# Kernel tuning notes

Hardware: AMD Instinct MI355X
Metric: run time of the kernel (lower is better)

Reference implementation:

```python
import jax, jax.numpy as jnp
import numpy as np

H = 1024        # hidden_dim
MD = 2048       # memory_dim
L = 16384       # memory length == max_length
N = 8           # head_N
# sys.float_info.min underflows to 0.0 in float32, exactly as in the torch
# original (python float * float32 tensor). Kept for faithfulness.
TINY = jnp.float32(2.2250738585072014e-308)


def setup_inputs() -> dict:
    key = jax.random.key(0)
    ks = jax.random.split(key, 12)
    s_h = 1.0 / np.sqrt(H)
    s_m = 1.0 / np.sqrt(MD)
    s_o = 1.0 / np.sqrt(2 * H)
    return {
        "x": jax.random.normal(ks[0], (1, 1, H), jnp.float32),
        "memory": jax.random.normal(ks[1], (L, MD), jnp.float32),
        "Wq": jax.random.uniform(ks[2], (H, H), jnp.float32, -s_h, s_h),
        "bq": jax.random.uniform(ks[3], (H,), jnp.float32, -s_h, s_h),
        "Wk": jax.random.uniform(ks[4], (H, MD), jnp.float32, -s_m, s_m),
        "bk": jax.random.uniform(ks[5], (H,), jnp.float32, -s_m, s_m),
        "Wv": jax.random.uniform(ks[6], (H, MD), jnp.float32, -s_m, s_m),
        "bv": jax.random.uniform(ks[7], (H,), jnp.float32, -s_m, s_m),
        "Wo": jax.random.uniform(ks[8], (H, 2 * H), jnp.float32, -s_o, s_o),
        "bo": jax.random.uniform(ks[9], (H,), jnp.float32, -s_o, s_o),
    }


def reference(x, memory, Wq, bq, Wk, bk, Wv, bv, Wo, bo):
    d = H // N  # per-head dim
    # Q: (1,H) -> (1,d,N) -> (N,1,d), scaled by d**-0.5
    q = x.reshape(1, -1) @ Wq.T + bq
    Q = q.reshape(1, d, N).transpose(2, 0, 1) * (d ** -0.5)
    # K: (L,H) -> (L,d,N) -> (N,d,L)
    K = (memory @ Wk.T + bk).reshape(-1, d, N).transpose(2, 1, 0)
    QK = jnp.einsum('nod,ndl->nol', Q, K)  # (N,1,L)
    # pad mask: 1 where the memory row sums to zero, else 0 (as in torch nonzero-set)
    any_zero = memory.sum(axis=1)
    pad_mask = (any_zero == 0).astype(QK.dtype)[None, None, :]
    QK = QK + pad_mask * TINY
    attn = jax.nn.softmax(QK, axis=-1)
    # V: (L,H) -> (L,d,N) -> (N,L,d)
    V = (memory @ Wv.T + bv).reshape(-1, d, N).transpose(2, 0, 1)
    feat = jnp.einsum('nol,nld->nod', attn, V)      # (N,1,d)
    feat = feat.transpose(1, 2, 0).reshape(1, 1, H)  # (1,1,H)
    ax = jnp.concatenate([x, feat], axis=-1)         # (1,1,2H)
    return jax.nn.relu(ax @ Wo.T + bo)
```

## Files before the change

### kernel.cpp

```cpp
#include <hip/hip_runtime.h>
#include <math.h>

#define HDIM  1024
#define MDIM  2048
#define RSQRT_D 0.08838834764831844f

#define OFF_W     0
#define OFF_BETA  16384
#define OFF_Z     16392
#define OFF_Q     16400
#define OFF_FEAT  17424
#define OFF_Y     18448
#define OFF_ZP    34832
#define OFF_YBUF  301072

__device__ __forceinline__ float dot4(float4 a, float4 b) {
  return a.x * b.x + a.y * b.y + a.z * b.z + a.w * b.w;
}
__device__ __forceinline__ void fma4(float4& acc, float s, float4 v) {
  acc.x = fmaf(s, v.x, acc.x); acc.y = fmaf(s, v.y, acc.y);
  acc.z = fmaf(s, v.z, acc.z); acc.w = fmaf(s, v.w, acc.w);
}
__device__ __forceinline__ void add4(float4& a, float4 v) {
  a.x += v.x; a.y += v.y; a.z += v.z; a.w += v.w;
}

__global__ __launch_bounds__(256) void kq(const float* __restrict__ x,
                                          const float* __restrict__ Wq,
                                          const float* __restrict__ bq,
                                          float* __restrict__ ws) {
  int tid = threadIdx.x, lane = tid & 63;
  int j = blockIdx.x * 4 + (tid >> 6);
  const float4* xr = (const float4*)x;
  const float4* wr = (const float4*)(Wq + (size_t)j * HDIM);
  float acc = 0.f;
#pragma unroll
  for (int i = 0; i < 4; ++i) {
    int idx = i * 64 + lane;
    acc += dot4(xr[idx], wr[idx]);
  }
#pragma unroll
  for (int off = 32; off; off >>= 1) acc += __shfl_xor(acc, off);
  if (lane == 0) ws[OFF_Q + j] = acc + bq[j];
  if (tid < 64) ws[OFF_W + blockIdx.x * 64 + tid] = 0.f;
}

__global__ __launch_bounds__(256) void kw(const float* __restrict__ Wk,
                                          const float* __restrict__ bk,
                                          float* __restrict__ ws) {
  __shared__ float lds[32];
  int tid = threadIdx.x;
  const float* q = ws + OFF_Q;
  if (blockIdx.x == 256) {
    float b = 0.f;
#pragma unroll
    for (int i = 0; i < 4; ++i) {
      int c = tid + 256 * i;
      b = fmaf(q[c], bk[c], b);
    }
    b += __shfl_xor(b, 8); b += __shfl_xor(b, 16); b += __shfl_xor(b, 32);
    if ((tid & 63) < 8) lds[(tid >> 6) * 8 + (tid & 7)] = b;
    __syncthreads();
    if (tid < 8)
      ws[OFF_BETA + tid] = lds[tid] + lds[8 + tid] + lds[16 + tid] + lds[24 + tid];
    return;
  }
  int mc = blockIdx.x & 7, cc = blockIdx.x >> 3;
  int m = mc * 256 + tid;
  float acc[8];
#pragma unroll
  for (int n = 0; n < 8; ++n) acc[n] = 0.f;
  int c0 = cc * 32;
#pragma unroll
  for (int cb = 0; cb < 32; cb += 8) {
#pragma unroll
    for (int u = 0; u < 8; ++u)
      acc[u] = fmaf(q[c0 + cb + u], Wk[(size_t)(c0 + cb + u) * MDIM + m], acc[u]);
  }
#pragma unroll
  for (int n = 0; n < 8; ++n) atomicAdd(&ws[OFF_W + n * MDIM + m], acc[n]);
}

__global__ __launch_bounds__(512, 4) void kab(const float* __restrict__ mem,
                                              float* __restrict__ ws) {
  __shared__ float4 wlds[4096];
  __shared__ __align__(16) float pp[256];
  __shared__ float zz[64];
  __shared__ float bb[8];
  int tid = threadIdx.x, lane = tid & 63, wv = tid >> 6;
  int bid = blockIdx.x;
  int r0 = bid * 32;

  const float4* wsrc = (const float4*)(ws + OFF_W);
#pragma unroll
  for (int k = 0; k < 8; ++k)
    wlds[k * 512 + tid] = wsrc[k * 512 + tid];
  if (tid < 8) bb[tid] = ws[OFF_BETA + tid];

  const float* rowp = mem + (size_t)(r0 + wv * 4) * MDIM;
  float4 mva[4], mvan[4], mvb[4];
#pragma unroll
  for (int i = 0; i < 4; ++i)
    mva[i] = *(const float4*)(rowp + (i * 64 + lane) * 4);
  __syncthreads();

  float zacc[8];
#pragma unroll
  for (int n = 0; n < 8; ++n) zacc[n] = 0.f;

#pragma unroll
  for (int rl = 0; rl < 4; ++rl) {
#pragma unroll
    for (int i = 0; i < 4; ++i)
      mvb[i] = *(const float4*)(rowp + 1024 + (i * 64 + lane) * 4);
    float acc[8];
#pragma unroll
    for (int n = 0; n < 8; ++n) acc[n] = 0.f;
#pragma unroll
    for (int pass = 0; pass < 4; ++pass) {
      int cq = pass * 64 + lane;
#pragma unroll
      for (int n = 0; n < 8; ++n) {
        float4 w4 = wlds[n * 512 + cq];
        acc[n] = fmaf(mva[pass].x, w4.x, acc[n]);
        acc[n] = fmaf(mva[pass].y, w4.y, acc[n]);
        acc[n] = fmaf(mva[pass].z, w4.z, acc[n]);
        acc[n] = fmaf(mva[pass].w, w4.w, acc[n]);
      }
    }
    if (rl < 3) {
#pragma unroll
      for (int i = 0; i < 4; ++i)
        mvan[i] = *(const float4*)(rowp + MDIM + (i * 64 + lane) * 4);
    }
#pragma unroll
    for (int pass = 0; pass < 4; ++pass) {
      int cq = 256 + pass * 64 + lane;
#pragma unroll
      for (int n = 0; n < 8; ++n) {
        float4 w4 = wlds[n * 512 + cq];
        acc[n] = fmaf(mvb[pass].x, w4.x, acc[n]);
        acc[n] = fmaf(mvb[pass].y, w4.y, acc[n]);
        acc[n] = fmaf(mvb[pass].z, w4.z, acc[n]);
        acc[n] = fmaf(mvb[pass].w, w4.w, acc[n]);
      }
    }
#pragma unroll
    for (int off = 1; off < 64; off <<= 1)
#pragma unroll
      for (int n = 0; n < 8; ++n)
        acc[n] += __shfl_xor(acc[n], off);
#pragma unroll
    for (int n = 0; n < 8; ++n) {
      float p = __expf((acc[n] + bb[n]) * RSQRT_D);
      zacc[n] += p;
      if (lane == 0) pp[(wv * 4 + rl) * 8 + n] = p;
    }
#pragma unroll
    for (int i = 0; i < 4; ++i) mva[i] = mvan[i];
    rowp += MDIM;
  }
  if (lane == 0) {
#pragma unroll
    for (int n = 0; n < 8; ++n) zz[wv * 8 + n] = zacc[n];
  }
  __syncthreads();
  if (tid < 8) {
    float z = 0.f;
#pragma unroll
    for (int w = 0; w < 8; ++w) z += zz[w * 8 + tid];
    ws[OFF_ZP + bid * 8 + tid] = z;
  }

  float4 acc4[8];
#pragma unroll
  for (int n = 0; n < 8; ++n) acc4[n] = make_float4(0.f, 0.f, 0.f, 0.f);
  const float* base = mem + (size_t)r0 * MDIM + tid * 4;
  const float4* pp4 = (const float4*)pp;
#pragma unroll 4
  for (int r = 0; r < 32; ++r) {
    float4 mv = *(const float4*)(base + (size_t)r * MDIM);
    float4 pA = pp4[r * 2], pB = pp4[r * 2 + 1];
    fma4(acc4[0], pA.x, mv); fma4(acc4[1], pA.y, mv);
    fma4(acc4[2], pA.z, mv); fma4(acc4[3], pA.w, mv);
    fma4(acc4[4], pB.x, mv); fma4(acc4[5], pB.y, mv);
    fma4(acc4[6], pB.z, mv); fma4(acc4[7], pB.w, mv);
  }
  float* yb = ws + OFF_YBUF + (size_t)bid * 16384 + tid * 4;
#pragma unroll
  for (int n = 0; n < 8; ++n)
    *(float4*)(yb + n * MDIM) = acc4[n];
}

__global__ __launch_bounds__(256) void ky(float* __restrict__ ws) {
  __shared__ __align__(16) float lds[96];
  int tid = threadIdx.x, lane = tid & 63, wv = tid >> 6;
  int bid = blockIdx.x;
  const float4* src = (const float4*)(ws + OFF_YBUF);
  int qd = bid * 4 + (tid & 3);
  int h = tid >> 2;
  float4 a = make_float4(0.f, 0.f, 0.f, 0.f);
#pragma unroll
  for (int i = 0; i < 8; ++i)
    add4(a, src[(size_t)(h + 64 * i) * 4096 + qd]);
#pragma unroll
  for (int off = 4; off < 64; off <<= 1) {
    a.x += __shfl_xor(a.x, off);
    a.y += __shfl_xor(a.y, off);
    a.z += __shfl_xor(a.z, off);
    a.w += __shfl_xor(a.w, off);
  }
  float4* sq = (float4*)lds;
  if (lane < 4) sq[wv * 4 + lane] = a;
  __syncthreads();
  if (tid < 4) {
    float4 s = sq[tid];
    add4(s, sq[4 + tid]); add4(s, sq[8 + tid]); add4(s, sq[12 + tid]);
    ((float4*)(ws + OFF_Y))[bid * 4 + tid] = s;
  }
  if (bid == 0) {
    int n = tid & 7;
    float z = 0.f;
#pragma unroll
    for (int i = 0; i < 16; ++i)
      z += ws[OFF_ZP + ((tid >> 3) + 32 * i) * 8 + n];
    z += __shfl_xor(z, 8); z += __shfl_xor(z, 16); z += __shfl_xor(z, 32);
    float* zzz = lds + 64;
    if (lane < 8) zzz[wv * 8 + lane] = z;
    __syncthreads();
    if (tid < 8)
      ws[OFF_Z + tid] = zzz[tid] + zzz[8 + tid] + zzz[16 + tid] + zzz[24 + tid];
  }
}

__global__ __launch_bounds__(256) void kf(const float* __restrict__ Wv,
                                          const float* __restrict__ bv,
                                          float* __restrict__ ws) {
  int tid = threadIdx.x, lane = tid & 63;
  int c = blockIdx.x * 4 + (tid >> 6);
  int n = c & 7;
  const float4* yb = (const float4*)(ws + OFF_Y + n * MDIM);
  const float4* wb = (const float4*)(Wv + (size_t)c * MDIM);
  float acc = 0.f;
#pragma unroll
  for (int s = 0; s < 8; ++s) {
    int idx = s * 64 + lane;
    acc += dot4(yb[idx], wb[idx]);
  }
#pragma unroll
  for (int off = 32; off; off >>= 1) acc += __shfl_xor(acc, off);
  if (lane == 0) ws[OFF_FEAT + c] = acc / ws[OFF_Z + n] + bv[c];
}

__global__ __launch_bounds__(256) void ko(const float* __restrict__ x,
                                          const float* __restrict__ Wo,
                                          const float* __restrict__ bo,
                                          const float* __restrict__ ws,
                                          float* __restrict__ out) {
  int tid = threadIdx.x, lane = tid & 63;
  int j = blockIdx.x * 4 + (tid >> 6);
  const float4* wb = (const float4*)(Wo + (size_t)j * 2048);
  const float4* xr = (const float4*)x;
  const float4* fr = (const float4*)(ws + OFF_FEAT);
  float acc = 0.f;
#pragma unroll
  for (int s = 0; s < 4; ++s) {
    int idx = s * 64 + lane;
    acc += dot4(xr[idx], wb[idx]);
    acc += dot4(fr[idx], wb[256 + idx]);
  }
#pragma unroll
  for (int off = 32; off; off >>= 1) acc += __shfl_xor(acc, off);
  if (lane == 0) out[j] = fmaxf(acc + bo[j], 0.f);
}

extern "C" void kernel_launch(void* const* d_in, const int* in_sizes, int n_in,
                              void* d_out, int out_size, void* d_ws, size_t ws_size,
                              hipStream_t stream) {
  const float* x   = (const float*)d_in[0];
  const float* mem = (const float*)d_in[1];
  const float* Wq  = (const float*)d_in[2];
  const float* bq  = (const float*)d_in[3];
  const float* Wk  = (const float*)d_in[4];
  const float* bk  = (const float*)d_in[5];
  const float* Wv  = (const float*)d_in[6];
  const float* bv  = (const float*)d_in[7];
  const float* Wo  = (const float*)d_in[8];
  const float* bo  = (const float*)d_in[9];
  float* ws  = (float*)d_ws;
  float* out = (float*)d_out;

  kq <<<256, 256, 0, stream>>>(x, Wq, bq, ws);
  kw <<<257, 256, 0, stream>>>(Wk, bk, ws);
  kab<<<512, 512, 0, stream>>>(mem, ws);
  ky <<<1024, 256, 0, stream>>>(ws);
  kf <<<256, 256, 0, stream>>>(Wv, bv, ws);
  ko <<<256, 256, 0, stream>>>(x, Wo, bo, ws, out);
}
```

Baseline: 262.9 us.

## Fuse Y-reduction, feature and output kernels with grid-wide atomic barriers

```diff
diff --git a/kernel.cpp b/kernel.cpp
--- a/kernel.cpp
+++ b/kernel.cpp
@@ -12,6 +12,7 @@
 #define OFF_FEAT  17424
 #define OFF_Y     18448
 #define OFF_ZP    34832
+#define OFF_BAR   38928
 #define OFF_YBUF  301072
 
 __device__ __forceinline__ float dot4(float4 a, float4 b) {
@@ -23,6 +24,17 @@
 }
 __device__ __forceinline__ void add4(float4& a, float4 v) {
   a.x += v.x; a.y += v.y; a.z += v.z; a.w += v.w;
+}
+
+__device__ __forceinline__ void kbar(unsigned* ctr, int tid) {
+  __syncthreads();
+  if (tid == 0) {
+    __hip_atomic_fetch_add(ctr, 1u, __ATOMIC_ACQ_REL, __HIP_MEMORY_SCOPE_AGENT);
+    while (__hip_atomic_load(ctr, __ATOMIC_RELAXED, __HIP_MEMORY_SCOPE_AGENT) < 256u)
+      __builtin_amdgcn_s_sleep(8);
+    (void)__hip_atomic_load(ctr, __ATOMIC_ACQUIRE, __HIP_MEMORY_SCOPE_AGENT);
+  }
+  __syncthreads();
 }
 
 __global__ __launch_bounds__(256) void kq(const float* __restrict__ x,
@@ -90,6 +102,8 @@
   int tid = threadIdx.x, lane = tid & 63, wv = tid >> 6;
   int bid = blockIdx.x;
   int r0 = bid * 32;
+
+  if (bid == 0 && tid < 2) ((unsigned*)(ws + OFF_BAR))[tid] = 0u;
 
   const float4* wsrc = (const float4*)(ws + OFF_W);
 #pragma unroll
@@ -192,31 +206,33 @@
     *(float4*)(yb + n * MDIM) = acc4[n];
 }
 
-__global__ __launch_bounds__(256) void ky(float* __restrict__ ws) {
-  __shared__ __align__(16) float lds[96];
+__global__ __launch_bounds__(256) void kyfo(const float* __restrict__ x,
+                                            const float* __restrict__ Wv,
+                                            const float* __restrict__ bv,
+                                            const float* __restrict__ Wo,
+                                            const float* __restrict__ bo,
+                                            float* __restrict__ ws,
+                                            float* __restrict__ out) {
+  __shared__ __align__(16) float lds[1056];
   int tid = threadIdx.x, lane = tid & 63, wv = tid >> 6;
   int bid = blockIdx.x;
-  const float4* src = (const float4*)(ws + OFF_YBUF);
-  int qd = bid * 4 + (tid & 3);
-  int h = tid >> 2;
-  float4 a = make_float4(0.f, 0.f, 0.f, 0.f);
-#pragma unroll
-  for (int i = 0; i < 8; ++i)
-    add4(a, src[(size_t)(h + 64 * i) * 4096 + qd]);
-#pragma unroll
-  for (int off = 4; off < 64; off <<= 1) {
-    a.x += __shfl_xor(a.x, off);
-    a.y += __shfl_xor(a.y, off);
-    a.z += __shfl_xor(a.z, off);
-    a.w += __shfl_xor(a.w, off);
-  }
-  float4* sq = (float4*)lds;
-  if (lane < 4) sq[wv * 4 + lane] = a;
-  __syncthreads();
-  if (tid < 4) {
-    float4 s = sq[tid];
-    add4(s, sq[4 + tid]); add4(s, sq[8 + tid]); add4(s, sq[12 + tid]);
-    ((float4*)(ws + OFF_Y))[bid * 4 + tid] = s;
+
+  {
+    float4* sA = (float4*)lds;
+    int quad = bid * 16 + (tid & 15);
+    int b0 = (tid >> 4) * 32;
+    const float4* src = (const float4*)(ws + OFF_YBUF);
+    float4 acc = make_float4(0.f, 0.f, 0.f, 0.f);
+    for (int b = b0; b < b0 + 32; ++b)
+      add4(acc, src[(size_t)b * 4096 + quad]);
+    sA[(tid & 15) * 16 + (tid >> 4)] = acc;
+    __syncthreads();
+    if (tid < 16) {
+      float4 s = sA[tid * 16];
+#pragma unroll
+      for (int j = 1; j < 16; ++j) add4(s, sA[tid * 16 + j]);
+      ((float4*)(ws + OFF_Y))[bid * 16 + tid] = s;
+    }
   }
   if (bid == 0) {
     int n = tid & 7;
@@ -225,53 +241,47 @@
     for (int i = 0; i < 16; ++i)
       z += ws[OFF_ZP + ((tid >> 3) + 32 * i) * 8 + n];
     z += __shfl_xor(z, 8); z += __shfl_xor(z, 16); z += __shfl_xor(z, 32);
-    float* zzz = lds + 64;
+    float* zzz = lds + 1024;
     if (lane < 8) zzz[wv * 8 + lane] = z;
     __syncthreads();
     if (tid < 8)
       ws[OFF_Z + tid] = zzz[tid] + zzz[8 + tid] + zzz[16 + tid] + zzz[24 + tid];
   }
-}
-
-__global__ __launch_bounds__(256) void kf(const float* __restrict__ Wv,
-                                          const float* __restrict__ bv,
-                                          float* __restrict__ ws) {
-  int tid = threadIdx.x, lane = tid & 63;
-  int c = blockIdx.x * 4 + (tid >> 6);
-  int n = c & 7;
-  const float4* yb = (const float4*)(ws + OFF_Y + n * MDIM);
-  const float4* wb = (const float4*)(Wv + (size_t)c * MDIM);
-  float acc = 0.f;
-#pragma unroll
-  for (int s = 0; s < 8; ++s) {
-    int idx = s * 64 + lane;
-    acc += dot4(yb[idx], wb[idx]);
-  }
-#pragma unroll
-  for (int off = 32; off; off >>= 1) acc += __shfl_xor(acc, off);
-  if (lane == 0) ws[OFF_FEAT + c] = acc / ws[OFF_Z + n] + bv[c];
-}
-
-__global__ __launch_bounds__(256) void ko(const float* __restrict__ x,
-                                          const float* __restrict__ Wo,
-                                          const float* __restrict__ bo,
-                                          const float* __restrict__ ws,
-                                          float* __restrict__ out) {
-  int tid = threadIdx.x, lane = tid & 63;
-  int j = blockIdx.x * 4 + (tid >> 6);
-  const float4* wb = (const float4*)(Wo + (size_t)j * 2048);
-  const float4* xr = (const float4*)x;
-  const float4* fr = (const float4*)(ws + OFF_FEAT);
-  float acc = 0.f;
-#pragma unroll
-  for (int s = 0; s < 4; ++s) {
-    int idx = s * 64 + lane;
-    acc += dot4(xr[idx], wb[idx]);
-    acc += dot4(fr[idx], wb[256 + idx]);
-  }
-#pragma unroll
-  for (int off = 32; off; off >>= 1) acc += __shfl_xor(acc, off);
-  if (lane == 0) out[j] = fmaxf(acc + bo[j], 0.f);
+  kbar((unsigned*)(ws + OFF_BAR), tid);
+
+  {
+    int c = bid * 4 + wv;
+    int n = c & 7;
+    const float4* yb = (const float4*)(ws + OFF_Y + n * MDIM);
+    const float4* wb = (const float4*)(Wv + (size_t)c * MDIM);
+    float acc = 0.f;
+#pragma unroll
+    for (int s = 0; s < 8; ++s) {
+      int idx = s * 64 + lane;
+      acc += dot4(yb[idx], wb[idx]);
+    }
+#pragma unroll
+    for (int off = 32; off; off >>= 1) acc += __shfl_xor(acc, off);
+    if (lane == 0) ws[OFF_FEAT + c] = acc / ws[OFF_Z + n] + bv[c];
+  }
+  kbar((unsigned*)(ws + OFF_BAR) + 1, tid);
+
+  {
+    int j = bid * 4 + wv;
+    const float4* wb = (const float4*)(Wo + (size_t)j * 2048);
+    const float4* xr = (const float4*)x;
+    const float4* fr = (const float4*)(ws + OFF_FEAT);
+    float acc = 0.f;
+#pragma unroll
+    for (int s = 0; s < 4; ++s) {
+      int idx = s * 64 + lane;
+      acc += dot4(xr[idx], wb[idx]);
+      acc += dot4(fr[idx], wb[256 + idx]);
+    }
+#pragma unroll
+    for (int off = 32; off; off >>= 1) acc += __shfl_xor(acc, off);
+    if (lane == 0) out[j] = fmaxf(acc + bo[j], 0.f);
+  }
 }
 
 extern "C" void kernel_launch(void* const* d_in, const int* in_sizes, int n_in,
@@ -290,10 +300,8 @@
   float* ws  = (float*)d_ws;
   float* out = (float*)d_out;
 
-  kq <<<256, 256, 0, stream>>>(x, Wq, bq, ws);
-  kw <<<257, 256, 0, stream>>>(Wk, bk, ws);
-  kab<<<512, 512, 0, stream>>>(mem, ws);
-  ky <<<1024, 256, 0, stream>>>(ws);
-  kf <<<256, 256, 0, stream>>>(Wv, bv, ws);
-  ko <<<256, 256, 0, stream>>>(x, Wo, bo, ws, out);
-}
+  kq  <<<256, 256, 0, stream>>>(x, Wq, bq, ws);
+  kw  <<<257, 256, 0, stream>>>(Wk, bk, ws);
+  kab <<<512, 512, 0, stream>>>(mem, ws);
+  kyfo<<<256, 256, 0, stream>>>(x, Wv, bv, Wo, bo, ws, out);
+}
```

Result: slower. 281.5 us (+7.1%).
